# Performance work log

Measured on AMD Instinct MI355X. Metric: run time of the kernel, lower is better.

## Reference

```python
import jax, jax.numpy as jnp
import numpy as np

B, T, H, D = 2, 2048, 8, 128
HID = H * D          # 1024
K_CONV = 4
EPS = 1e-5


def causal_dwconv(x, w, b):
    # x: [B,T,C], w: [C,K], b: [C]
    # torch Conv1d(groups=C, padding=K-1) followed by [..., :T] == left-padded causal depthwise conv
    K = w.shape[1]
    Tx = x.shape[1]
    xp = jnp.pad(x, ((0, 0), (K - 1, 0), (0, 0)))
    acc = jnp.zeros_like(x)
    for j in range(K):  # tiny fixed loop over kernel taps
        acc = acc + xp[:, j:j + Tx, :] * w[:, j]
    return acc + b


def setup_inputs() -> dict:
    key = jax.random.key(0)
    ks = jax.random.split(key, 16)
    s = 0.02
    inp = {
        'x':   jax.random.normal(ks[0], (B, T, HID), jnp.float32),
        'Wq':  s * jax.random.normal(ks[1], (HID, H * D), jnp.float32),
        'Wk':  s * jax.random.normal(ks[2], (HID, H * D), jnp.float32),
        'Wv':  s * jax.random.normal(ks[3], (HID, H * D), jnp.float32),
        'Wa':  s * jax.random.normal(ks[4], (HID, H * D), jnp.float32),
        'ba':  jnp.zeros((H * D,), jnp.float32),
        'Wb':  s * jax.random.normal(ks[5], (HID, H), jnp.float32),
        'bb':  jnp.zeros((H,), jnp.float32),
        'Wg':  s * jax.random.normal(ks[6], (HID, H * D), jnp.float32),
        'Wo':  s * jax.random.normal(ks[7], (H * D, HID), jnp.float32),
        'cqw': s * jax.random.normal(ks[8], (H * D, K_CONV), jnp.float32),
        'cqb': jnp.zeros((H * D,), jnp.float32),
        'ckw': s * jax.random.normal(ks[9], (H * D, K_CONV), jnp.float32),
        'ckb': jnp.zeros((H * D,), jnp.float32),
        'cvw': s * jax.random.normal(ks[10], (H * D, K_CONV), jnp.float32),
        'cvb': jnp.zeros((H * D,), jnp.float32),
        'ln_g': jnp.ones((D,), jnp.float32),
        'ln_b': jnp.zeros((D,), jnp.float32),
    }
    return inp


def reference(x, Wq, Wk, Wv, Wa, ba, Wb, bb, Wg, Wo,
              cqw, cqb, ckw, ckb, cvw, cvb, ln_g, ln_b):
    Bx, Tx, _ = x.shape
    q = x @ Wq
    k = x @ Wk
    v = x @ Wv
    q = jax.nn.silu(causal_dwconv(q, cqw, cqb))
    k = jax.nn.silu(causal_dwconv(k, ckw, ckb))
    v = jax.nn.silu(causal_dwconv(v, cvw, cvb))
    q = q.reshape(Bx, Tx, H, D)
    k = k.reshape(Bx, Tx, H, D) * (D ** -0.5)   # k scaled by head_dim_qk**-0.5
    v = v.reshape(Bx, Tx, H, D)
    a = jax.nn.sigmoid(x @ Wa + ba).reshape(Bx, Tx, H, D)
    beta = jax.nn.sigmoid(x @ Wb + bb)           # [B,T,H]

    # delta-rule recurrent scan; state S: [B,H,Dv,Dk]
    def step(S, inp):
        q_t, k_t, v_t, a_t, b_t = inp            # [B,H,D] / beta [B,H]
        delta = jnp.einsum('bhvk,bhk->bhv', S, k_t)
        err = delta - v_t
        S = a_t[..., None] * S - (b_t[..., None] * err)[..., None] * k_t[:, :, None, :]
        o_t = jnp.einsum('bhvk,bhk->bhv', S, q_t)
        return S, o_t

    tfirst = lambda z: jnp.moveaxis(z, 1, 0)     # [B,T,...] -> [T,B,...]
    S0 = jnp.zeros((Bx, H, D, D), x.dtype)
    _, o = jax.lax.scan(step, S0, (tfirst(q), tfirst(k), tfirst(v), tfirst(a), tfirst(beta)))
    o = jnp.moveaxis(o, 0, 1)                    # [B,T,H,D]

    # LayerNorm over head_dim_v
    mu = o.mean(-1, keepdims=True)
    var = ((o - mu) ** 2).mean(-1, keepdims=True)
    o = (o - mu) * jax.lax.rsqrt(var + EPS) * ln_g + ln_b

    g = jax.nn.sigmoid(x @ Wg).reshape(Bx, Tx, H, D)
    o = (o * g).reshape(Bx, Tx, H * D)
    return o @ Wo
```

## Files before the change

### kernel.cpp

```cpp
#include <hip/hip_runtime.h>
#include <hip/hip_bf16.h>
#include <cstdint>
#include <cstddef>

#define BATCH 2
#define TLEN  2048
#define NHEAD 8
#define HD    128
#define HIDN  1024
#define MTOT  4096
#define MAT_ELEMS 1048576
#define XELEMS 4194304
#define SCAN_C 32
#define NCH    64
#define SSC  1024.0f
#define ISSC 0.0009765625f

typedef _Float16 f16;
typedef _Float16 f16x2 __attribute__((ext_vector_type(2)));
typedef _Float16 f16x8 __attribute__((ext_vector_type(8)));
typedef float    f32x4 __attribute__((ext_vector_type(4)));

__device__ __forceinline__ float sigmoidf_(float v) { return 1.0f / (1.0f + __expf(-v)); }

__device__ __forceinline__ float fdot2_(f16x2 a, f16x2 b, float c)
{
#if __has_builtin(__builtin_amdgcn_fdot2)
    return __builtin_amdgcn_fdot2(a, b, c, false);
#else
    return fmaf((float)a.x, (float)b.x, fmaf((float)a.y, (float)b.y, c));
#endif
}

__device__ __forceinline__ void gload_lds16(const f16* g, f16* l)
{
    __builtin_amdgcn_global_load_lds(
        (const __attribute__((address_space(1))) uint32_t*)(g),
        (__attribute__((address_space(3))) uint32_t*)(l), 16, 0, 0);
}

__global__ __launch_bounds__(256) void convert_x_kernel(const float* __restrict__ x,
                                                        f16* __restrict__ x16)
{
    int i = (blockIdx.x * 256 + threadIdx.x) * 4;
    float4 v = *(const float4*)(x + i);
    union { f16 h[4]; uint2 u; } pk;
    pk.h[0] = (f16)v.x; pk.h[1] = (f16)v.y; pk.h[2] = (f16)v.z; pk.h[3] = (f16)v.w;
    *(uint2*)(x16 + i) = pk.u;
}

__global__ __launch_bounds__(256) void transpose_convert_kernel(
    const float* __restrict__ Wq, const float* __restrict__ Wk, const float* __restrict__ Wv,
    const float* __restrict__ Wa, const float* __restrict__ Wg, const float* __restrict__ Wo,
    f16* __restrict__ WT)
{
    __shared__ float tile[32][33];
    int mat = blockIdx.z;
    const float* W = (mat == 0) ? Wq : (mat == 1) ? Wk : (mat == 2) ? Wv
                   : (mat == 3) ? Wa : (mat == 4) ? Wg : Wo;
    int k0 = blockIdx.y * 32, n0 = blockIdx.x * 32;
    int tr = threadIdx.x >> 3;
    int tc = (threadIdx.x & 7) * 4;
    float4 vin = *(const float4*)(W + (size_t)(k0 + tr) * HIDN + n0 + tc);
    tile[tr][tc + 0] = vin.x; tile[tr][tc + 1] = vin.y;
    tile[tr][tc + 2] = vin.z; tile[tr][tc + 3] = vin.w;
    __syncthreads();
    f16* dst = WT + (size_t)(mat * HIDN + n0 + tr) * HIDN + k0 + tc;
    union { f16 h[4]; uint2 u; } pk;
    pk.h[0] = (f16)tile[tc + 0][tr]; pk.h[1] = (f16)tile[tc + 1][tr];
    pk.h[2] = (f16)tile[tc + 2][tr]; pk.h[3] = (f16)tile[tc + 3][tr];
    *(uint2*)dst = pk.u;
}

template <int MODE>
__global__ __launch_bounds__(256) void gemm_f16(
    const f16* __restrict__ A, const f16* __restrict__ BT,
    float* __restrict__ out_f32,
    f16* __restrict__ qkv_hat, float* __restrict__ a_buf, f16* __restrict__ g16,
    const float* __restrict__ ba)
{
    __shared__ __align__(16) f16 As[128][40];
    __shared__ __align__(16) f16 Bs[128][40];
    int m0 = blockIdx.y * 128;
    int n0 = blockIdx.x * 128;
    int tid = threadIdx.x;
    int w = tid >> 6, lane = tid & 63;
    int L16 = lane & 15, quad = lane >> 4;
    int wm = (w >> 1) * 64, wn = (w & 1) * 64;

    f32x4 acc[4][4];
#pragma unroll
    for (int i = 0; i < 4; ++i)
#pragma unroll
        for (int j = 0; j < 4; ++j) acc[i][j] = (f32x4){0.f, 0.f, 0.f, 0.f};

    int ldr = tid >> 2;
    int ldc = (tid & 3) * 8;

    for (int k0 = 0; k0 < 1024; k0 += 32) {
        uint4 a0 = *(const uint4*)(A + (size_t)(m0 + ldr) * HIDN + k0 + ldc);
        uint4 a1 = *(const uint4*)(A + (size_t)(m0 + ldr + 64) * HIDN + k0 + ldc);
        uint4 b0 = *(const uint4*)(BT + (size_t)(n0 + ldr) * HIDN + k0 + ldc);
        uint4 b1 = *(const uint4*)(BT + (size_t)(n0 + ldr + 64) * HIDN + k0 + ldc);
        __syncthreads();
        *(uint4*)(&As[ldr][ldc]) = a0;
        *(uint4*)(&As[ldr + 64][ldc]) = a1;
        *(uint4*)(&Bs[ldr][ldc]) = b0;
        *(uint4*)(&Bs[ldr + 64][ldc]) = b1;
        __syncthreads();
        f16x8 af[4], bf[4];
#pragma unroll
        for (int i = 0; i < 4; ++i) {
            af[i] = *(const f16x8*)(&As[wm + i * 16 + L16][quad * 8]);
            bf[i] = *(const f16x8*)(&Bs[wn + i * 16 + L16][quad * 8]);
        }
#pragma unroll
        for (int i = 0; i < 4; ++i)
#pragma unroll
            for (int j = 0; j < 4; ++j)
                acc[i][j] = __builtin_amdgcn_mfma_f32_16x16x32_f16(af[i], bf[j], acc[i][j], 0, 0, 0);
    }

#pragma unroll
    for (int i = 0; i < 4; ++i) {
#pragma unroll
        for (int j = 0; j < 4; ++j) {
            f32x4 c = acc[i][j];
            int mbase = m0 + wm + i * 16 + quad * 4;
            int n = n0 + wn + j * 16 + L16;
            if (MODE == 1) {
#pragma unroll
                for (int r = 0; r < 4; ++r)
                    out_f32[(size_t)(mbase + r) * HIDN + n] = c[r];
            } else {
                int mat = n >> 10;
                int nn = n & 1023;
                if (mat < 3) {
#pragma unroll
                    for (int r = 0; r < 4; ++r)
                        qkv_hat[(size_t)mat * XELEMS + (size_t)(mbase + r) * HIDN + nn] = (f16)c[r];
                } else if (mat == 3) {
                    float bav = ba[nn];
#pragma unroll
                    for (int r = 0; r < 4; ++r)
                        a_buf[(size_t)(mbase + r) * HIDN + nn] = sigmoidf_(c[r] + bav);
                } else {
#pragma unroll
                    for (int r = 0; r < 4; ++r)
                        g16[(size_t)(mbase + r) * HIDN + nn] = (f16)sigmoidf_(c[r]);
                }
            }
        }
    }
}

__global__ __launch_bounds__(256) void beta_kernel(const float* __restrict__ x,
                                                   const float* __restrict__ Wb,
                                                   const float* __restrict__ bb,
                                                   float* __restrict__ beta_buf)
{
    int row = blockIdx.x;
    int h = threadIdx.x >> 5, lane = threadIdx.x & 31;
    const float* xr = x + (size_t)row * HIDN;
    float part = 0.f;
    for (int i = lane; i < HIDN; i += 32)
        part += xr[i] * Wb[i * NHEAD + h];
#pragma unroll
    for (int m = 1; m <= 16; m <<= 1) part += __shfl_xor(part, m);
    if (lane == 0)
        beta_buf[(size_t)row * NHEAD + h] = sigmoidf_(part + bb[h]);
}

__global__ __launch_bounds__(256) void conv_silu_kernel(
    const f16* __restrict__ qkv_hat,
    const float* __restrict__ cqw, const float* __restrict__ cqb,
    const float* __restrict__ ckw, const float* __restrict__ ckb,
    const float* __restrict__ cvw, const float* __restrict__ cvb,
    f16* __restrict__ qkv16)
{
    int z = blockIdx.y;
    int row = blockIdx.x;
    int tloc = row & (TLEN - 1);
    int c4 = threadIdx.x * 4;
    const f16* src = qkv_hat + (size_t)z * XELEMS;
    const float* w  = (z == 0) ? cqw : (z == 1) ? ckw : cvw;
    const float* bi = (z == 0) ? cqb : (z == 1) ? ckb : cvb;

    float xv[4][4];
#pragma unroll
    for (int j = 0; j < 4; ++j) {
        int tt = tloc - 3 + j;
        if (tt >= 0) {
            const f16* p = src + (size_t)(row - 3 + j) * HIDN + c4;
            xv[j][0] = (float)p[0]; xv[j][1] = (float)p[1];
            xv[j][2] = (float)p[2]; xv[j][3] = (float)p[3];
        } else {
            xv[j][0] = xv[j][1] = xv[j][2] = xv[j][3] = 0.f;
        }
    }
    float scale = (z == 1) ? 0.08838834764831845f : 1.0f;
    union { f16 h[4]; uint2 u; } pk;
#pragma unroll
    for (int cc = 0; cc < 4; ++cc) {
        float4 wc = *(const float4*)(w + (size_t)(c4 + cc) * 4);
        float acc = bi[c4 + cc] + wc.x * xv[0][cc] + wc.y * xv[1][cc]
                                 + wc.z * xv[2][cc] + wc.w * xv[3][cc];
        pk.h[cc] = (f16)(acc * sigmoidf_(acc) * scale);
    }
    *(uint2*)(qkv16 + (size_t)z * XELEMS + (size_t)row * HIDN + c4) = pk.u;
}

__global__ __launch_bounds__(64) void gram_kernel(
    const f16* __restrict__ q16, const f16* __restrict__ k16,
    f16* __restrict__ G_g, f16* __restrict__ KQ_g,
    f16* __restrict__ Gx_g, f16* __restrict__ Qx_g, f16* __restrict__ KT_g)
{
    int ch = blockIdx.x;
    int bh = blockIdx.y;
    int b = bh >> 3, h = bh & 7;
    int lane = threadIdx.x;
    int L16 = lane & 15, quad = lane >> 4;
    size_t rowbase = (size_t)(b * TLEN) * HIDN + h * HD;
    int t0 = ch * SCAN_C;
    bool hasNext = (ch + 1 < NCH);

    union ZU { uint4 u; f16x8 v; };
    ZU zz; zz.u = (uint4){0, 0, 0, 0};

    f16x8 kc[2][4], qc[2][4], kn[2][4], qn[2][4];
#pragma unroll
    for (int nt = 0; nt < 2; ++nt)
#pragma unroll
        for (int kk = 0; kk < 4; ++kk) {
            size_t g = rowbase + (size_t)(t0 + nt * 16 + L16) * HIDN + kk * 32 + quad * 8;
            kc[nt][kk] = *(const f16x8*)(k16 + g);
            qc[nt][kk] = *(const f16x8*)(q16 + g);
            if (hasNext) {
                kn[nt][kk] = *(const f16x8*)(k16 + g + (size_t)SCAN_C * HIDN);
                qn[nt][kk] = *(const f16x8*)(q16 + g + (size_t)SCAN_C * HIDN);
            } else {
                kn[nt][kk] = zz.v; qn[nt][kk] = zz.v;
            }
        }

    f32x4 aG[2][2], aKQ[2][2], aGx[2][2], aQx[2][2];
#pragma unroll
    for (int i = 0; i < 2; ++i)
#pragma unroll
        for (int j = 0; j < 2; ++j) {
            aG[i][j] = (f32x4){0, 0, 0, 0}; aKQ[i][j] = (f32x4){0, 0, 0, 0};
            aGx[i][j] = (f32x4){0, 0, 0, 0}; aQx[i][j] = (f32x4){0, 0, 0, 0};
        }
#pragma unroll
    for (int kk = 0; kk < 4; ++kk)
#pragma unroll
        for (int mt = 0; mt < 2; ++mt)
#pragma unroll
            for (int nt = 0; nt < 2; ++nt) {
                aG[mt][nt]  = __builtin_amdgcn_mfma_f32_16x16x32_f16(kc[mt][kk], kc[nt][kk], aG[mt][nt], 0, 0, 0);
                aKQ[mt][nt] = __builtin_amdgcn_mfma_f32_16x16x32_f16(kc[mt][kk], qc[nt][kk], aKQ[mt][nt], 0, 0, 0);
                aGx[mt][nt] = __builtin_amdgcn_mfma_f32_16x16x32_f16(kc[mt][kk], kn[nt][kk], aGx[mt][nt], 0, 0, 0);
                aQx[mt][nt] = __builtin_amdgcn_mfma_f32_16x16x32_f16(kc[mt][kk], qn[nt][kk], aQx[mt][nt], 0, 0, 0);
            }

    size_t gb = ((size_t)bh * NCH + ch) * 1024;
#pragma unroll
    for (int nt = 0; nt < 2; ++nt) {
        int t = nt * 16 + L16;
#pragma unroll
        for (int mt = 0; mt < 2; ++mt) {
            union { f16 e[4]; uint2 u2; } pg, pq, px, py;
#pragma unroll
            for (int r = 0; r < 4; ++r) {
                pg.e[r] = (f16)aG[mt][nt][r];
                pq.e[r] = (f16)aKQ[mt][nt][r];
                px.e[r] = (f16)aGx[mt][nt][r];
                py.e[r] = (f16)aQx[mt][nt][r];
            }
            *(uint2*)(G_g  + gb + t * 32 + mt * 16 + quad * 4) = pg.u2;
            *(uint2*)(KQ_g + gb + t * 32 + mt * 16 + quad * 4) = pq.u2;
            *(uint2*)(Gx_g + gb + t * 32 + mt * 16 + quad * 4) = px.u2;
            *(uint2*)(Qx_g + gb + t * 32 + mt * 16 + quad * 4) = py.u2;
        }
    }
    size_t kb = ((size_t)bh * NCH + ch) * 4096;
#pragma unroll
    for (int nt = 0; nt < 2; ++nt) {
        int t = nt * 16 + L16;
#pragma unroll
        for (int kk = 0; kk < 4; ++kk)
#pragma unroll
            for (int j = 0; j < 8; ++j) {
                int k = kk * 32 + quad * 8 + j;
                KT_g[kb + (size_t)k * 32 + t] = kc[nt][kk][j];
            }
    }
}

__global__ __launch_bounds__(128, 1) void scan2_kernel(
    const f16* __restrict__ q16, const f16* __restrict__ k16, const f16* __restrict__ v16,
    const float* __restrict__ a_buf, const float* __restrict__ beta_buf,
    const f16* __restrict__ G_g, const f16* __restrict__ KQ_g,
    const f16* __restrict__ Gx_g, const f16* __restrict__ Qx_g, const f16* __restrict__ KT_g,
    float* __restrict__ o_buf)
{
    __shared__ __align__(16) float Sp[16 * 132];
    __shared__ __align__(16) f16   Sp16[16 * 136];
    __shared__ __align__(16) f16   KT_lds2[2][4096];
    __shared__ __align__(16) f16   G_lds[2][1024];
    __shared__ __align__(16) f16   Q_lds[2][1024];
    __shared__ __align__(16) f16   Gx_lds[2][1024];
    __shared__ __align__(16) f16   Qx_lds[2][1024];
    __shared__ __align__(16) float skv[2][16 * 34];
    __shared__ __align__(16) float sqv[2][16 * 34];
    __shared__ __align__(16) float avb[2][16 * 68];
    __shared__ __align__(16) float Bts[2][32];
    __shared__ __align__(16) f16   c16s[2][16 * 40];
    __shared__ __align__(16) float PCs[2][16];

    const int tid = threadIdx.x;
    const int wid = tid >> 6;
    const int lane = tid & 63;
    const int L16 = lane & 15, quad = lane >> 4;
    const int vl = lane >> 2, li = lane & 3;
    const int t_av = lane >> 1, halfsel = lane & 1;

    const int bh = blockIdx.x;
    const int b = bh >> 3, h = bh & 7;
    const int v0 = blockIdx.y * 16;
    const size_t rowbase = (size_t)(b * TLEN) * HIDN + h * HD;
    const size_t gmatbase = (size_t)bh * NCH;

    {
        for (int i = tid; i < 16 * 132; i += 128) Sp[i] = 0.f;
        uint32_t* z;
        z = (uint32_t*)Sp16;    for (int i = tid; i < 16 * 136 / 2; i += 128) z[i] = 0u;
        z = (uint32_t*)KT_lds2; for (int i = tid; i < 2 * 4096 / 2; i += 128) z[i] = 0u;
        z = (uint32_t*)G_lds;   for (int i = tid; i < 1024;          i += 128) z[i] = 0u;
        z = (uint32_t*)Q_lds;   for (int i = tid; i < 1024;          i += 128) z[i] = 0u;
        z = (uint32_t*)Gx_lds;  for (int i = tid; i < 1024;          i += 128) z[i] = 0u;
        z = (uint32_t*)Qx_lds;  for (int i = tid; i < 1024;          i += 128) z[i] = 0u;
        z = (uint32_t*)skv;     for (int i = tid; i < 2 * 16 * 34;   i += 128) z[i] = 0u;
        z = (uint32_t*)sqv;     for (int i = tid; i < 2 * 16 * 34;   i += 128) z[i] = 0u;
        z = (uint32_t*)avb;     for (int i = tid; i < 2 * 16 * 68;   i += 128) z[i] = 0u;
        z = (uint32_t*)Bts;     for (int i = tid; i < 2 * 32;        i += 128) z[i] = 0u;
        z = (uint32_t*)c16s;    for (int i = tid; i < 2 * 16 * 40 / 2; i += 128) z[i] = 0u;
        z = (uint32_t*)PCs;     for (int i = tid; i < 2 * 16;        i += 128) z[i] = 0u;
    }
    __syncthreads();

    if (wid == 1) {
        f16x8 kfA[2][4], qfA[2][4], kfB[2][4], qfB[2][4];

        {
            size_t gb0 = gmatbase * 1024;
            *(uint4*)(&G_lds[0][lane * 16])     = *(const uint4*)(G_g  + gb0 + lane * 16);
            *(uint4*)(&G_lds[0][lane * 16 + 8]) = *(const uint4*)(G_g  + gb0 + lane * 16 + 8);
            *(uint4*)(&Q_lds[0][lane * 16])     = *(const uint4*)(KQ_g + gb0 + lane * 16);
            *(uint4*)(&Q_lds[0][lane * 16 + 8]) = *(const uint4*)(KQ_g + gb0 + lane * 16 + 8);
            size_t ga = rowbase + (size_t)t_av * HIDN + v0 + halfsel * 8;
            float4 ar0 = *(const float4*)(a_buf + ga);
            float4 ar1 = *(const float4*)(a_buf + ga + 4);
            uint4  vr  = *(const uint4*)(v16 + ga);
            float betr = beta_buf[((size_t)(b * TLEN) + t_av) * NHEAD + h];
            const f16* vh = (const f16*)&vr;
            const float* aa0 = (const float*)&ar0;
            const float* aa1 = (const float*)&ar1;
#pragma unroll
            for (int e = 0; e < 4; ++e) {
                float2 wv; wv.x = aa0[e]; wv.y = betr * (float)vh[e];
                *(float2*)(&avb[0][(halfsel * 8 + e) * 68 + 2 * t_av]) = wv;
                float2 wu; wu.x = aa1[e]; wu.y = betr * (float)vh[4 + e];
                *(float2*)(&avb[0][(halfsel * 8 + 4 + e) * 68 + 2 * t_av]) = wu;
            }
            if (halfsel == 0) Bts[0][t_av] = betr;
        }
        __syncthreads();

#define DO_UPDATE_MM(KF, QF)                                                        \
        if (ch >= 1 && ch <= NCH - 2) {                                             \
            f16x8 ca = *(const f16x8*)(&c16s[np][L16 * 40 + quad * 8]);             \
            float pc = PCs[np][L16];                                                \
            _Pragma("unroll")                                                       \
            for (int kt = 0; kt < 8; ++kt) {                                        \
                f16x8 bu = *(const f16x8*)(&KT_lds2[p][(kt * 16 + L16) * 32 + quad * 8]); \
                f32x4 d = __builtin_amdgcn_mfma_f32_16x16x32_f16(bu, ca, (f32x4){0, 0, 0, 0}, 0, 0, 0); \
                int idx = L16 * 132 + kt * 16 + quad * 4;                           \
                float4 s = *(const float4*)(&Sp[idx]);                              \
                s.x = fmaf(pc, s.x, d[0]);                                          \
                s.y = fmaf(pc, s.y, d[1]);                                          \
                s.z = fmaf(pc, s.z, d[2]);                                          \
                s.w = fmaf(pc, s.w, d[3]);                                          \
                *(float4*)(&Sp[idx]) = s;                                           \
                union { f16 e[4]; uint2 u2; } ph;                                   \
                ph.e[0] = (f16)s.x; ph.e[1] = (f16)s.y;                             \
                ph.e[2] = (f16)s.z; ph.e[3] = (f16)s.w;                             \
                *(uint2*)(&Sp16[L16 * 136 + kt * 16 + quad * 4]) = ph.u2;           \
            }                                                                       \
            f32x4 accK[2], accQ[2];                                                 \
            accK[0] = (f32x4){0, 0, 0, 0}; accK[1] = (f32x4){0, 0, 0, 0};           \
            accQ[0] = (f32x4){0, 0, 0, 0}; accQ[1] = (f32x4){0, 0, 0, 0};           \
            _Pragma("unroll")                                                       \
            for (int kk = 0; kk < 4; ++kk) {                                        \
                f16x8 sf = *(const f16x8*)(&Sp16[L16 * 136 + kk * 32 + quad * 8]);  \
                _Pragma("unroll")                                                   \
                for (int nt = 0; nt < 2; ++nt) {                                    \
                    accK[nt] = __builtin_amdgcn_mfma_f32_16x16x32_f16(sf, KF[nt][kk], accK[nt], 0, 0, 0); \
                    accQ[nt] = __builtin_amdgcn_mfma_f32_16x16x32_f16(sf, QF[nt][kk], accQ[nt], 0, 0, 0); \
                }                                                                   \
            }                                                                       \
            _Pragma("unroll")                                                       \
            for (int nt = 0; nt < 2; ++nt) {                                        \
                int t = nt * 16 + L16;                                              \
                _Pragma("unroll")                                                   \
                for (int r = 0; r < 4; ++r) {                                       \
                    skv[np][(quad * 4 + r) * 34 + t] = accK[nt][r];                 \
                    sqv[np][(quad * 4 + r) * 34 + t] = accQ[nt][r];                 \
                }                                                                   \
            }                                                                       \
        }

#define DO_PREFETCH(KF, QF)                                                         \
        if (ch <= NCH - 3) {                                                        \
            int tp = (ch + 2) * SCAN_C;                                             \
            _Pragma("unroll")                                                       \
            for (int nt = 0; nt < 2; ++nt)                                          \
                _Pragma("unroll")                                                   \
                for (int kk = 0; kk < 4; ++kk) {                                    \
                    size_t g = rowbase + (size_t)(tp + nt * 16 + L16) * HIDN + kk * 32 + quad * 8; \
                    KF[nt][kk] = *(const f16x8*)(k16 + g);                          \
                    QF[nt][kk] = *(const f16x8*)(q16 + g);                          \
                }                                                                   \
        }

        for (int ch = 0; ch < NCH; ++ch) {
            const int p = ch & 1;
            const int np = p ^ 1;
            const bool haveNext = (ch + 1 < NCH);

            float4 ar0, ar1; uint4 vr; float betr = 0.f;
            if (haveNext) {
                size_t gbn = (gmatbase + ch + 1) * 1024;
                size_t gbc = (gmatbase + ch) * 1024;
                const f16* gG = G_g  + gbn + lane * 8;
                const f16* gQ = KQ_g + gbn + lane * 8;
                const f16* gX = Gx_g + gbc + lane * 8;
                const f16* gY = Qx_g + gbc + lane * 8;
                gload_lds16(gG,       &G_lds[np][0]);
                gload_lds16(gG + 512, &G_lds[np][512]);
                gload_lds16(gQ,       &Q_lds[np][0]);
                gload_lds16(gQ + 512, &Q_lds[np][512]);
                gload_lds16(gX,       &Gx_lds[np][0]);
                gload_lds16(gX + 512, &Gx_lds[np][512]);
                gload_lds16(gY,       &Qx_lds[np][0]);
                gload_lds16(gY + 512, &Qx_lds[np][512]);
                const f16* gK = KT_g + (gmatbase + ch) * 4096 + lane * 8;
#pragma unroll
                for (int i = 0; i < 8; ++i)
                    gload_lds16(gK + i * 512, &KT_lds2[np][i * 512]);
                int tn = (ch + 1) * SCAN_C;
                size_t ga = rowbase + (size_t)(tn + t_av) * HIDN + v0 + halfsel * 8;
                ar0 = *(const float4*)(a_buf + ga);
                ar1 = *(const float4*)(a_buf + ga + 4);
                vr  = *(const uint4*)(v16 + ga);
                betr = beta_buf[((size_t)(b * TLEN) + tn + t_av) * NHEAD + h];
            }

            if ((ch & 1) == 0) { DO_UPDATE_MM(kfA, qfA) DO_PREFETCH(kfB, qfB) }
            else               { DO_UPDATE_MM(kfB, qfB) DO_PREFETCH(kfA, qfA) }

            if (haveNext) {
                const f16* vh = (const f16*)&vr;
                const float* aa0 = (const float*)&ar0;
                const float* aa1 = (const float*)&ar1;
#pragma unroll
                for (int e = 0; e < 4; ++e) {
                    float2 wv; wv.x = aa0[e]; wv.y = betr * (float)vh[e];
                    *(float2*)(&avb[np][(halfsel * 8 + e) * 68 + 2 * t_av]) = wv;
                    float2 wu; wu.x = aa1[e]; wu.y = betr * (float)vh[4 + e];
                    *(float2*)(&avb[np][(halfsel * 8 + 4 + e) * 68 + 2 * t_av]) = wu;
                }
                if (halfsel == 0) Bts[np][t_av] = betr;
            }
            __syncthreads();
        }
#undef DO_UPDATE_MM
#undef DO_PREFETCH
    } else {
        __builtin_amdgcn_s_setprio(1);
        __syncthreads();
        const size_t obase = rowbase + v0 + vl;

        for (int ch = 0; ch < NCH; ++ch) {
            const int p = ch & 1;
            const int np = p ^ 1;
            const int t0 = ch * SCAN_C;

            {
                f16x8 caf = *(const f16x8*)(&c16s[np][L16 * 40 + quad * 8]);
                f32x4 fK[2], fQ[2];
#pragma unroll
                for (int nt = 0; nt < 2; ++nt) {
                    f16x8 bx = *(const f16x8*)(&Gx_lds[p][(nt * 16 + L16) * 32 + quad * 8]);
                    f16x8 by = *(const f16x8*)(&Qx_lds[p][(nt * 16 + L16) * 32 + quad * 8]);
                    fK[nt] = __builtin_amdgcn_mfma_f32_16x16x32_f16(caf, bx, (f32x4){0, 0, 0, 0}, 0, 0, 0);
                    fQ[nt] = __builtin_amdgcn_mfma_f32_16x16x32_f16(caf, by, (f32x4){0, 0, 0, 0}, 0, 0, 0);
                }
#pragma unroll
                for (int r = 0; r < 4; ++r) {
                    int vv = quad * 4 + r;
                    float Pv = PCs[np][vv];
#pragma unroll
                    for (int nt = 0; nt < 2; ++nt) {
                        int t = nt * 16 + L16;
                        skv[p][vv * 34 + t] = fmaf(Pv, skv[p][vv * 34 + t], fK[nt][r]);
                        sqv[p][vv * 34 + t] = fmaf(Pv, sqv[p][vv * 34 + t], fQ[nt][r]);
                    }
                }
            }

            {
                f16x2 c0, c1, c2, c3;
                c0.x = (f16)0.f; c0.y = (f16)0.f; c1 = c0; c2 = c0; c3 = c0;
                float P = 1.f;
                union RowU { uint4 u4; f16x2 h2[4]; };
#pragma unroll
                for (int t = 0; t < SCAN_C; t += 2) {
                    RowU g0u, g1u, h0u, h1u;
                    g0u.u4 = *(const uint4*)(&G_lds[p][t * 32 + li * 8]);
                    g1u.u4 = *(const uint4*)(&G_lds[p][(t + 1) * 32 + li * 8]);
                    h0u.u4 = *(const uint4*)(&Q_lds[p][t * 32 + li * 8]);
                    h1u.u4 = *(const uint4*)(&Q_lds[p][(t + 1) * 32 + li * 8]);
                    float2 skp = *(const float2*)(&skv[p][vl * 34 + t]);
                    float2 sqp = *(const float2*)(&sqv[p][vl * 34 + t]);
                    float4 ab4 = *(const float4*)(&avb[p][vl * 68 + 2 * t]);
                    float2 btp = *(const float2*)(&Bts[p][t]);
                    float kq00 = (float)Q_lds[p][t * 32 + t];
                    f16x2 dq  = *(const f16x2*)(&Q_lds[p][(t + 1) * 32 + t]);
                    float g01 = (float)G_lds[p][(t + 1) * 32 + t];

                    float pG  = fdot2_(c0, g0u.h2[0], fdot2_(c1, g0u.h2[1], 0.f))
                              + fdot2_(c2, g0u.h2[2], fdot2_(c3, g0u.h2[3], 0.f));
                    float pG1 = fdot2_(c0, g1u.h2[0], fdot2_(c1, g1u.h2[1], 0.f))
                              + fdot2_(c2, g1u.h2[2], fdot2_(c3, g1u.h2[3], 0.f));
                    float pO  = fdot2_(c0, h0u.h2[0], fdot2_(c1, h0u.h2[1], 0.f))
                              + fdot2_(c2, h0u.h2[2], fdot2_(c3, h0u.h2[3], 0.f));
                    float pO1 = fdot2_(c0, h1u.h2[0], fdot2_(c1, h1u.h2[1], 0.f))
                              + fdot2_(c2, h1u.h2[2], fdot2_(c3, h1u.h2[3], 0.f));
                    int tmp;
                    tmp = __builtin_amdgcn_update_dpp(0, __float_as_int(pG),  0xB1, 0xF, 0xF, true); pG  += __int_as_float(tmp);
                    tmp = __builtin_amdgcn_update_dpp(0, __float_as_int(pG1), 0xB1, 0xF, 0xF, true); pG1 += __int_as_float(tmp);
                    tmp = __builtin_amdgcn_update_dpp(0, __float_as_int(pO),  0xB1, 0xF, 0xF, true); pO  += __int_as_float(tmp);
                    tmp = __builtin_amdgcn_update_dpp(0, __float_as_int(pO1), 0xB1, 0xF, 0xF, true); pO1 += __int_as_float(tmp);
                    tmp = __builtin_amdgcn_update_dpp(0, __float_as_int(pG),  0x4E, 0xF, 0xF, true); pG  += __int_as_float(tmp);
                    tmp = __builtin_amdgcn_update_dpp(0, __float_as_int(pG1), 0x4E, 0xF, 0xF, true); pG1 += __int_as_float(tmp);
                    tmp = __builtin_amdgcn_update_dpp(0, __float_as_int(pO),  0x4E, 0xF, 0xF, true); pO  += __int_as_float(tmp);
                    tmp = __builtin_amdgcn_update_dpp(0, __float_as_int(pO1), 0x4E, 0xF, 0xF, true); pO1 += __int_as_float(tmp);

                    float a0 = ab4.x, bv0 = ab4.y, a1 = ab4.z, bv1 = ab4.w;
                    float bt0 = btp.x, bt1 = btp.y;
                    float sk0 = skp.x * ISSC, sk1 = skp.y * ISSC;
                    float sq0 = sqp.x * ISSC, sq1 = sqp.y * ISSC;
                    float kq01 = (float)dq.x, kq11 = (float)dq.y;

                    float x0 = fmaf(P, sk0, pG);
                    float u0 = fmaf(-bt0, x0, bv0);
                    float P0 = P * a0;
                    float o0 = fmaf(a0, pO, u0 * kq00);
                    o0 = fmaf(P0, sq0, o0);
                    float accGv = fmaf(a0, pG1, u0 * g01);
                    float x1 = fmaf(P0, sk1, accGv);
                    float u1 = fmaf(-bt1, x1, bv1);
                    float P1 = P0 * a1;
                    float accOv = fmaf(a0, pO1, u0 * kq01);
                    float o1 = fmaf(a1, accOv, u1 * kq11);
                    o1 = fmaf(P1, sq1, o1);

                    float aa = a0 * a1;
                    f16 aah = (f16)aa;
                    f16x2 aa2; aa2.x = aah; aa2.y = aah;
                    c0 *= aa2; c1 *= aa2; c2 *= aa2; c3 *= aa2;
                    if (li == (t >> 3)) {
                        f16x2 un; un.x = (f16)(u0 * a1); un.y = (f16)u1;
                        int sel = (t & 7) >> 1;
                        if (sel == 0) c0 = un; else if (sel == 1) c1 = un;
                        else if (sel == 2) c2 = un; else c3 = un;
                    }
                    P = P1;
                    if (li == 0) {
                        o_buf[obase + (size_t)(t0 + t) * HIDN]     = o0;
                        o_buf[obase + (size_t)(t0 + t + 1) * HIDN] = o1;
                    }
                }
                f16 s16 = (f16)SSC;
                f16x2 ss2; ss2.x = s16; ss2.y = s16;
                union { f16x2 h2[4]; uint4 u4; } pc;
                pc.h2[0] = c0 * ss2; pc.h2[1] = c1 * ss2; pc.h2[2] = c2 * ss2; pc.h2[3] = c3 * ss2;
                *(uint4*)(&c16s[p][vl * 40 + li * 8]) = pc.u4;
                if (li == 0) PCs[p][vl] = P;
            }
            __syncthreads();
        }
    }
}

__global__ __launch_bounds__(256) void ln_gate_kernel(
    const float* __restrict__ o_buf, const f16* __restrict__ g16,
    const float* __restrict__ lng, const float* __restrict__ lnb,
    f16* __restrict__ og16)
{
    int row = blockIdx.x;
    int h = threadIdx.x >> 5, lane = threadIdx.x & 31;
    size_t base = (size_t)row * HIDN + h * HD + lane * 4;
    float4 x = *(const float4*)(o_buf + base);
    float s  = x.x + x.y + x.z + x.w;
    float sq = x.x * x.x + x.y * x.y + x.z * x.z + x.w * x.w;
#pragma unroll
    for (int m = 1; m <= 16; m <<= 1) {
        s  += __shfl_xor(s, m);
        sq += __shfl_xor(sq, m);
    }
    float mu  = s * (1.0f / 128.0f);
    float var = sq * (1.0f / 128.0f) - mu * mu;
    float inv = 1.0f / sqrtf(var + 1e-5f);
    int d = lane * 4;
    const float* xp = (const float*)&x;
    union { f16 h4[4]; uint2 u; } pk;
#pragma unroll
    for (int j = 0; j < 4; ++j) {
        float on = (xp[j] - mu) * inv * lng[d + j] + lnb[d + j];
        pk.h4[j] = (f16)(on * (float)g16[base + j]);
    }
    *(uint2*)(og16 + base) = pk.u;
}

extern "C" void kernel_launch(void* const* d_in, const int* in_sizes, int n_in,
                              void* d_out, int out_size, void* d_ws, size_t ws_size,
                              hipStream_t stream)
{
    (void)in_sizes; (void)n_in; (void)out_size; (void)ws_size;
    const float* x   = (const float*)d_in[0];
    const float* Wq  = (const float*)d_in[1];
    const float* Wk  = (const float*)d_in[2];
    const float* Wv  = (const float*)d_in[3];
    const float* Wa  = (const float*)d_in[4];
    const float* ba  = (const float*)d_in[5];
    const float* Wb  = (const float*)d_in[6];
    const float* bb  = (const float*)d_in[7];
    const float* Wg  = (const float*)d_in[8];
    const float* Wo  = (const float*)d_in[9];
    const float* cqw = (const float*)d_in[10];
    const float* cqb = (const float*)d_in[11];
    const float* ckw = (const float*)d_in[12];
    const float* ckb = (const float*)d_in[13];
    const float* cvw = (const float*)d_in[14];
    const float* cvb = (const float*)d_in[15];
    const float* lng = (const float*)d_in[16];
    const float* lnb = (const float*)d_in[17];
    float* out = (float*)d_out;

    char* ws = (char*)d_ws;
    f16*   x16      = (f16*)(ws + 0);
    f16*   WT       = (f16*)(ws + 8388608);
    f16*   qkvh     = (f16*)(ws + 20971520);
    f16*   qkv16    = (f16*)(ws + 46137344);
    float* a_buf    = (float*)(ws + 96468992);
    f16*   g16      = (f16*)(ws + 113246208);
    float* beta_buf = (float*)(ws + 121634816);
    float* o_buf    = (float*)(ws + 121765888);
    f16*   og16     = (f16*)(ws + 138543104);

    f16* G_g  = qkvh;
    f16* KQ_g = qkvh + 1048576;
    f16* Gx_g = qkvh + 2097152;
    f16* Qx_g = qkvh + 3145728;
    f16* KT_g = qkvh + 4194304;

    convert_x_kernel<<<dim3(4096), dim3(256), 0, stream>>>(x, x16);
    transpose_convert_kernel<<<dim3(32, 32, 6), dim3(256), 0, stream>>>(Wq, Wk, Wv, Wa, Wg, Wo, WT);
    gemm_f16<0><<<dim3(40, 32), dim3(256), 0, stream>>>(x16, WT, nullptr, qkvh, a_buf, g16, ba);
    beta_kernel<<<dim3(4096), dim3(256), 0, stream>>>(x, Wb, bb, beta_buf);
    conv_silu_kernel<<<dim3(4096, 3), dim3(256), 0, stream>>>(qkvh, cqw, cqb, ckw, ckb, cvw, cvb, qkv16);
    gram_kernel<<<dim3(NCH, 16), dim3(64), 0, stream>>>(
        qkv16, qkv16 + XELEMS, G_g, KQ_g, Gx_g, Qx_g, KT_g);
    scan2_kernel<<<dim3(16, 8), dim3(128), 0, stream>>>(
        qkv16, qkv16 + XELEMS, qkv16 + 2 * (size_t)XELEMS, a_buf, beta_buf,
        G_g, KQ_g, Gx_g, Qx_g, KT_g, o_buf);
    ln_gate_kernel<<<dim3(4096), dim3(256), 0, stream>>>(o_buf, g16, lng, lnb, og16);
    gemm_f16<1><<<dim3(8, 32), dim3(256), 0, stream>>>(og16, WT + 5 * (size_t)MAT_ELEMS, out,
                                                       nullptr, nullptr, nullptr, nullptr);
}
```

Measured before the change: 576.0 us.

## Stage scan outputs in LDS and software-pipeline solve-loop LDS loads

```diff
diff --git a/kernel.cpp b/kernel.cpp
--- a/kernel.cpp
+++ b/kernel.cpp
@@ -317,6 +317,7 @@
     __shared__ __align__(16) float Bts[2][32];
     __shared__ __align__(16) f16   c16s[2][16 * 40];
     __shared__ __align__(16) float PCs[2][16];
+    __shared__ __align__(16) float o_lds[2][16][34];
 
     const int tid = threadIdx.x;
     const int wid = tid >> 6;
@@ -466,8 +467,26 @@
                 betr = beta_buf[((size_t)(b * TLEN) + tn + t_av) * NHEAD + h];
             }
 
-            if ((ch & 1) == 0) { DO_UPDATE_MM(kfA, qfA) DO_PREFETCH(kfB, qfB) }
-            else               { DO_UPDATE_MM(kfB, qfB) DO_PREFETCH(kfA, qfA) }
+            if ((ch & 1) == 0) { DO_PREFETCH(kfB, qfB) }
+            else               { DO_PREFETCH(kfA, qfA) }
+
+            if (ch >= 1) {
+                const int fp = (ch - 1) & 1;
+                const int tprev = (ch - 1) * SCAN_C;
+                const int tt = lane >> 1;
+                const int hh = (lane & 1) * 8;
+                float v8[8];
+#pragma unroll
+                for (int j = 0; j < 8; ++j) v8[j] = o_lds[fp][hh + j][tt];
+                float4 f0; f0.x = v8[0]; f0.y = v8[1]; f0.z = v8[2]; f0.w = v8[3];
+                float4 f1; f1.x = v8[4]; f1.y = v8[5]; f1.z = v8[6]; f1.w = v8[7];
+                size_t ob = rowbase + (size_t)(tprev + tt) * HIDN + v0 + hh;
+                *(float4*)(o_buf + ob)     = f0;
+                *(float4*)(o_buf + ob + 4) = f1;
+            }
+
+            if ((ch & 1) == 0) { DO_UPDATE_MM(kfA, qfA) }
+            else               { DO_UPDATE_MM(kfB, qfB) }
 
             if (haveNext) {
                 const f16* vh = (const f16*)&vr;
@@ -486,15 +505,28 @@
         }
 #undef DO_UPDATE_MM
 #undef DO_PREFETCH
+
+        {
+            const int fp = (NCH - 1) & 1;
+            const int tprev = (NCH - 1) * SCAN_C;
+            const int tt = lane >> 1;
+            const int hh = (lane & 1) * 8;
+            float v8[8];
+#pragma unroll
+            for (int j = 0; j < 8; ++j) v8[j] = o_lds[fp][hh + j][tt];
+            float4 f0; f0.x = v8[0]; f0.y = v8[1]; f0.z = v8[2]; f0.w = v8[3];
+            float4 f1; f1.x = v8[4]; f1.y = v8[5]; f1.z = v8[6]; f1.w = v8[7];
+            size_t ob = rowbase + (size_t)(tprev + tt) * HIDN + v0 + hh;
+            *(float4*)(o_buf + ob)     = f0;
+            *(float4*)(o_buf + ob + 4) = f1;
+        }
     } else {
         __builtin_amdgcn_s_setprio(1);
         __syncthreads();
-        const size_t obase = rowbase + v0 + vl;
 
         for (int ch = 0; ch < NCH; ++ch) {
             const int p = ch & 1;
             const int np = p ^ 1;
-            const int t0 = ch * SCAN_C;
 
             {
                 f16x8 caf = *(const f16x8*)(&c16s[np][L16 * 40 + quad * 8]);
@@ -524,20 +556,41 @@
                 c0.x = (f16)0.f; c0.y = (f16)0.f; c1 = c0; c2 = c0; c3 = c0;
                 float P = 1.f;
                 union RowU { uint4 u4; f16x2 h2[4]; };
+
+                uint4  pg0[2], pg1[2], ph0[2], ph1[2];
+                float2 pskp[2], psqp[2], pbtp[2];
+                float4 pab4[2];
+                float  pkq00[2], pg01[2];
+                f16x2  pdq[2];
+
+#define SOLVE_LD(SL, TT)                                                            \
+                {                                                                   \
+                    pg0[SL] = *(const uint4*)(&G_lds[p][(TT) * 32 + li * 8]);       \
+                    pg1[SL] = *(const uint4*)(&G_lds[p][((TT) + 1) * 32 + li * 8]); \
+                    ph0[SL] = *(const uint4*)(&Q_lds[p][(TT) * 32 + li * 8]);       \
+                    ph1[SL] = *(const uint4*)(&Q_lds[p][((TT) + 1) * 32 + li * 8]); \
+                    pskp[SL] = *(const float2*)(&skv[p][vl * 34 + (TT)]);           \
+                    psqp[SL] = *(const float2*)(&sqv[p][vl * 34 + (TT)]);           \
+                    pab4[SL] = *(const float4*)(&avb[p][vl * 68 + 2 * (TT)]);       \
+                    pbtp[SL] = *(const float2*)(&Bts[p][(TT)]);                     \
+                    pkq00[SL] = (float)Q_lds[p][(TT) * 32 + (TT)];                  \
+                    pdq[SL]  = *(const f16x2*)(&Q_lds[p][((TT) + 1) * 32 + (TT)]);  \
+                    pg01[SL] = (float)G_lds[p][((TT) + 1) * 32 + (TT)];             \
+                }
+
+                SOLVE_LD(0, 0)
+                SOLVE_LD(1, 2)
 #pragma unroll
                 for (int t = 0; t < SCAN_C; t += 2) {
+                    const int sl = (t >> 1) & 1;
                     RowU g0u, g1u, h0u, h1u;
-                    g0u.u4 = *(const uint4*)(&G_lds[p][t * 32 + li * 8]);
-                    g1u.u4 = *(const uint4*)(&G_lds[p][(t + 1) * 32 + li * 8]);
-                    h0u.u4 = *(const uint4*)(&Q_lds[p][t * 32 + li * 8]);
-                    h1u.u4 = *(const uint4*)(&Q_lds[p][(t + 1) * 32 + li * 8]);
-                    float2 skp = *(const float2*)(&skv[p][vl * 34 + t]);
-                    float2 sqp = *(const float2*)(&sqv[p][vl * 34 + t]);
-                    float4 ab4 = *(const float4*)(&avb[p][vl * 68 + 2 * t]);
-                    float2 btp = *(const float2*)(&Bts[p][t]);
-                    float kq00 = (float)Q_lds[p][t * 32 + t];
-                    f16x2 dq  = *(const f16x2*)(&Q_lds[p][(t + 1) * 32 + t]);
-                    float g01 = (float)G_lds[p][(t + 1) * 32 + t];
+                    g0u.u4 = pg0[sl]; g1u.u4 = pg1[sl];
+                    h0u.u4 = ph0[sl]; h1u.u4 = ph1[sl];
+                    float2 skp = pskp[sl], sqp = psqp[sl], btp = pbtp[sl];
+                    float4 ab4 = pab4[sl];
+                    float kq00 = pkq00[sl], g01 = pg01[sl];
+                    f16x2 dq = pdq[sl];
+                    if (t + 4 < SCAN_C) SOLVE_LD(sl, t + 4)
 
                     float pG  = fdot2_(c0, g0u.h2[0], fdot2_(c1, g0u.h2[1], 0.f))
                               + fdot2_(c2, g0u.h2[2], fdot2_(c3, g0u.h2[3], 0.f));
@@ -588,10 +641,11 @@
                     }
                     P = P1;
                     if (li == 0) {
-                        o_buf[obase + (size_t)(t0 + t) * HIDN]     = o0;
-                        o_buf[obase + (size_t)(t0 + t + 1) * HIDN] = o1;
+                        float2 o2; o2.x = o0; o2.y = o1;
+                        *(float2*)(&o_lds[p][vl][t]) = o2;
                     }
                 }
+#undef SOLVE_LD
                 f16 s16 = (f16)SSC;
                 f16x2 ss2; ss2.x = s16; ss2.y = s16;
                 union { f16x2 h2[4]; uint4 u4; } pc;
```

New measurement: 525.8 us. 8.7% less time.
